# Performance work log

Hardware: AMD Instinct MI355X
Metric: run time of the kernel (lower is better)

## Reference

```python
import jax, jax.numpy as jnp
import numpy as np

NUM_EMBEDDINGS = 8192
EMBEDDING_DIM = 64
N_VOXELS = 32768


def setup_inputs() -> dict:
    key = jax.random.key(0)
    k1, k2 = jax.random.split(key)
    z = jax.random.normal(k1, (N_VOXELS, EMBEDDING_DIM), dtype=jnp.float32)
    codebook = jax.random.normal(k2, (NUM_EMBEDDINGS, EMBEDDING_DIM), dtype=jnp.float32)
    return {"z": z, "codebook": codebook}


def reference(z, codebook):
    # Squared euclidean distances [N, K]; argmin is identical to argmin of cdist.
    # d2 = ||z||^2 - 2 z E^T + ||E||^2
    z_sq = jnp.sum(z * z, axis=1, keepdims=True)            # [N, 1]
    e_sq = jnp.sum(codebook * codebook, axis=1)              # [K]
    d2 = z_sq - 2.0 * (z @ codebook.T) + e_sq[None, :]       # [N, K]
    encoding_indices = jnp.argmin(d2, axis=1)                # [N] int

    quantized_feats = codebook[encoding_indices]             # [N, D] gather

    sg = jax.lax.stop_gradient
    commitment_loss = jnp.mean((z - sg(quantized_feats)) ** 2)
    vq_loss = jnp.mean((quantized_feats - sg(z)) ** 2)

    # Straight-through estimator
    quantized = z + sg(quantized_feats - z)                  # [N, D]

    return quantized, vq_loss, commitment_loss, encoding_indices
```

## Files before the change

### kernel.cpp

```cpp
#include <hip/hip_runtime.h>
#include <math.h>

#define N_VOX 32768
#define N_EMB 8192
#define DIM 64
#define NCHUNK 8
#define CODES_PER_CHUNK (N_EMB / NCHUNK)
#define TILES_PER_CHUNK (CODES_PER_CHUNK / 32)
#define NTILES (N_EMB / 32)
#define TILE_BYTES 8192
#define CHUNK_BYTES (TILES_PER_CHUNK * TILE_BYTES)

typedef _Float16 half8 __attribute__((ext_vector_type(8)));
typedef float floatx16 __attribute__((ext_vector_type(16)));

#define FP16_MIN_NORMAL 6.1035156e-5f
#define LO_SCALE 2048.0f

__global__ __launch_bounds__(64) void cbprep_kernel(const float* __restrict__ cb,
                                                    char* __restrict__ stream,
                                                    float* __restrict__ c0arr) {
    int l    = threadIdx.x;
    int m    = l & 31;
    int kg   = l >> 5;
    int tile = blockIdx.x;
    char* tbase = stream + (size_t)tile * TILE_BYTES;
    int code = tile * 32 + m;

    float ss = 0.f;
    #pragma unroll
    for (int o = 0; o < 4; ++o) {
        const float* p = cb + (size_t)code * DIM + o * 16 + kg * 8;
        half8 h, lo;
        #pragma unroll
        for (int j = 0; j < 8; ++j) {
            float x = p[j];
            ss = fmaf(x, x, ss);
            _Float16 hi = (_Float16)x;
            float hf = (float)hi;
            if (fabsf(hf) < FP16_MIN_NORMAL) { hi = (_Float16)0.f; hf = 0.f; }
            h[j]  = hi;
            lo[j] = (_Float16)((x - hf) * LO_SCALE);
        }
        *(half8*)(tbase +        o * 1024 + l * 16) = h;
        *(half8*)(tbase + 4096 + o * 1024 + l * 16) = lo;
    }
    ss += __shfl_xor(ss, 32, 64);
    if (kg == 0)
        c0arr[code] = -1024.0f * ss;
}

__global__ __launch_bounds__(512) void scan_kernel(const float* __restrict__ z,
                                                   const char* __restrict__ stream,
                                                   const float* __restrict__ c0arr,
                                                   float* __restrict__ cand_val,
                                                   int* __restrict__ cand_idx) {
    __shared__ __align__(16) char lds[2 * TILE_BYTES];
    int tid   = threadIdx.x;
    int l     = tid & 63;
    int w     = tid >> 6;
    int chunk = blockIdx.x & (NCHUNK - 1);
    int rg    = blockIdx.x >> 3;
    int m     = l & 31;
    int kg    = l >> 5;
    int rowBase = rg * 256 + w * 32;

    half8 zh[4], zl[4], zhs[4];
    const float* zrow = z + (size_t)(rowBase + m) * DIM + kg * 8;
    #pragma unroll
    for (int o = 0; o < 4; ++o) {
        const float* p = zrow + o * 16;
        #pragma unroll
        for (int j = 0; j < 8; ++j) {
            float x = p[j];
            _Float16 hi = (_Float16)x;
            float hf = (float)hi;
            if (fabsf(hf) < FP16_MIN_NORMAL) { hi = (_Float16)0.f; hf = 0.f; }
            zh[o][j] = hi;
            zl[o][j] = (_Float16)((x - hf) * LO_SCALE);
        }
        zhs[o] = zh[o] * (_Float16)2048.0f;
    }

    const char*  sbase = stream + (size_t)chunk * CHUNK_BYTES;
    const float* c0p   = c0arr + chunk * CODES_PER_CHUNK;

    float best[16];
    int   bt[16];
    #pragma unroll
    for (int i = 0; i < 16; ++i) { best[i] = -3.4e38f; bt[i] = 0; }

#define STAGE(gt, lb)                                                              \
    do {                                                                           \
        const char* _g = (gt) + w * 1024 + l * 16;                                 \
        char*       _d = (lb) + w * 1024 + l * 16;                                 \
        __builtin_amdgcn_global_load_lds(                                          \
            (const __attribute__((address_space(1))) void*)_g,                     \
            (__attribute__((address_space(3))) void*)_d, 16, 0, 0);                \
    } while (0)

    STAGE(sbase, lds);
    float c0 = c0p[m];
    __syncthreads();

    for (int t = 0; t < TILES_PER_CHUNK; ++t) {
        if (t + 1 < TILES_PER_CHUNK)
            STAGE(sbase + (size_t)(t + 1) * TILE_BYTES, lds + ((t + 1) & 1) * TILE_BYTES);
        float c0n = (t + 1 < TILES_PER_CHUNK) ? c0p[(t + 1) * 32 + m] : 0.f;

        const char* lb = lds + (t & 1) * TILE_BYTES;
        half8 bh[4], bl[4];
        #pragma unroll
        for (int o = 0; o < 4; ++o) {
            bh[o] = *(const half8*)(lb +        o * 1024 + l * 16);
            bl[o] = *(const half8*)(lb + 4096 + o * 1024 + l * 16);
        }

        floatx16 acc;
        #pragma unroll
        for (int i = 0; i < 16; ++i) acc[i] = c0;
        #pragma unroll
        for (int o = 0; o < 4; ++o) {
            acc = __builtin_amdgcn_mfma_f32_32x32x16_f16(zhs[o], bh[o], acc, 0, 0, 0);
            acc = __builtin_amdgcn_mfma_f32_32x32x16_f16(zl[o],  bh[o], acc, 0, 0, 0);
            acc = __builtin_amdgcn_mfma_f32_32x32x16_f16(zh[o],  bl[o], acc, 0, 0, 0);
        }
        #pragma unroll
        for (int i = 0; i < 16; ++i)
            if (acc[i] > best[i]) { best[i] = acc[i]; bt[i] = t; }

        c0 = c0n;
        __syncthreads();
    }
#undef STAGE

    #pragma unroll
    for (int i = 0; i < 16; ++i) {
        float v  = best[i];
        int   id = bt[i] * 32 + m;
        #pragma unroll
        for (int off = 1; off < 32; off <<= 1) {
            float ov = __shfl_xor(v, off, 64);
            int   oi = __shfl_xor(id, off, 64);
            if (ov > v || (ov == v && oi < id)) { v = ov; id = oi; }
        }
        if (m == 0) {
            int row = rowBase + (i & 3) + 8 * (i >> 2) + 4 * kg;
            cand_val[chunk * N_VOX + row] = v;
            cand_idx[chunk * N_VOX + row] = chunk * CODES_PER_CHUNK + id;
        }
    }
}

__global__ __launch_bounds__(256) void finalize_kernel(const float* __restrict__ z,
                                                       const float* __restrict__ cb,
                                                       const float* __restrict__ cand_val,
                                                       const int* __restrict__ cand_idx,
                                                       float* __restrict__ out,
                                                       float* __restrict__ partials) {
    int g    = blockIdx.x * 256 + threadIdx.x;
    int row  = g >> 3;
    int c    = g & 7;

    float v  = cand_val[c * N_VOX + row];
    int   id = cand_idx[c * N_VOX + row];
    #pragma unroll
    for (int off = 1; off < 8; off <<= 1) {
        float ov = __shfl_xor(v, off, 8);
        int   oi = __shfl_xor(id, off, 8);
        if (ov > v || (ov == v && oi < id)) { v = ov; id = oi; }
    }

    if (c == 0)
        out[(size_t)N_VOX * DIM + 2 + row] = (float)id;

    const float4* zp = (const float4*)(z  + (size_t)row * DIM + c * 8);
    const float4* qp = (const float4*)(cb + (size_t)id  * DIM + c * 8);
    float4*       op = (float4*)(out + (size_t)row * DIM + c * 8);
    float ss = 0.f;
    #pragma unroll
    for (int d = 0; d < 2; ++d) {
        float4 zt = zp[d], qt = qp[d];
        float dx = qt.x - zt.x, dy = qt.y - zt.y;
        float dz = qt.z - zt.z, dw = qt.w - zt.w;
        float4 o;
        o.x = zt.x + dx; o.y = zt.y + dy;
        o.z = zt.z + dz; o.w = zt.w + dw;
        op[d] = o;
        ss += dx*dx + dy*dy + dz*dz + dw*dw;
    }

    __shared__ float red[256];
    red[threadIdx.x] = ss;
    __syncthreads();
    #pragma unroll
    for (int s = 128; s > 0; s >>= 1) {
        if (threadIdx.x < s) red[threadIdx.x] += red[threadIdx.x + s];
        __syncthreads();
    }
    if (threadIdx.x == 0) partials[blockIdx.x] = red[0];
}

__global__ __launch_bounds__(256) void loss_kernel(const float* __restrict__ partials,
                                                   float* __restrict__ out) {
    __shared__ float red[256];
    red[threadIdx.x] = (partials[threadIdx.x]       + partials[threadIdx.x + 256])
                     + (partials[threadIdx.x + 512] + partials[threadIdx.x + 768]);
    __syncthreads();
    #pragma unroll
    for (int st = 128; st > 0; st >>= 1) {
        if (threadIdx.x < st) red[threadIdx.x] += red[threadIdx.x + st];
        __syncthreads();
    }
    if (threadIdx.x == 0) {
        float mean = red[0] / (float)((size_t)N_VOX * DIM);
        out[(size_t)N_VOX * DIM + 0] = mean;
        out[(size_t)N_VOX * DIM + 1] = mean;
    }
}

extern "C" void kernel_launch(void* const* d_in, const int* in_sizes, int n_in,
                              void* d_out, int out_size, void* d_ws, size_t ws_size,
                              hipStream_t stream) {
    const float* z  = (const float*)d_in[0];
    const float* cb = (const float*)d_in[1];
    float* out = (float*)d_out;

    char*  bstream  = (char*)d_ws;
    float* c0arr    = (float*)(bstream + (size_t)NTILES * TILE_BYTES);
    float* cand_val = c0arr + N_EMB;
    int*   cand_idx = (int*)(cand_val + (size_t)NCHUNK * N_VOX);
    float* partials = (float*)(cand_idx + (size_t)NCHUNK * N_VOX);

    cbprep_kernel  <<<dim3(NTILES), dim3(64), 0, stream>>>(cb, bstream, c0arr);
    scan_kernel    <<<dim3((N_VOX / 256) * NCHUNK), dim3(512), 0, stream>>>(z, bstream, c0arr, cand_val, cand_idx);
    finalize_kernel<<<dim3(N_VOX * 8 / 256), dim3(256), 0, stream>>>(z, cb, cand_val, cand_idx, out, partials);
    loss_kernel    <<<1, 256, 0, stream>>>(partials, out);
}
```

Before: 175.9 us.

## Deepen codebook tile pipeline to four LDS buffers and preload norms

The scan kernel moves from double-buffered to quad-buffered LDS staging with a prefetch distance of three tiles. It uses explicit vmcnt waits plus a single barrier per iteration in place of the trailing __syncthreads. Per-chunk codebook norms are loaded into LDS once instead of fetched from global memory each tile. The codebook prep kernel spreads the four 16-element slices across four wavefronts with an LDS reduction, aiming at more memory parallelism in that small kernel. LDS use per block grows to about 36 KB, which may lower occupancy. The hand-written waitcnt logic depends on the exact number of outstanding loads, which the z loads or c0 loads could disturb.

```diff
diff --git a/kernel.cpp b/kernel.cpp
--- a/kernel.cpp
+++ b/kernel.cpp
@@ -17,37 +17,43 @@
 #define FP16_MIN_NORMAL 6.1035156e-5f
 #define LO_SCALE 2048.0f
 
-__global__ __launch_bounds__(64) void cbprep_kernel(const float* __restrict__ cb,
-                                                    char* __restrict__ stream,
-                                                    float* __restrict__ c0arr) {
-    int l    = threadIdx.x;
+__global__ __launch_bounds__(256) void cbprep_kernel(const float* __restrict__ cb,
+                                                     char* __restrict__ stream,
+                                                     float* __restrict__ c0arr) {
+    __shared__ float red[256];
+    int tid  = threadIdx.x;
+    int l    = tid & 63;
+    int o    = tid >> 6;
     int m    = l & 31;
     int kg   = l >> 5;
     int tile = blockIdx.x;
     char* tbase = stream + (size_t)tile * TILE_BYTES;
     int code = tile * 32 + m;
 
+    const float* p = cb + (size_t)code * DIM + o * 16 + kg * 8;
     float ss = 0.f;
-    #pragma unroll
-    for (int o = 0; o < 4; ++o) {
-        const float* p = cb + (size_t)code * DIM + o * 16 + kg * 8;
-        half8 h, lo;
-        #pragma unroll
-        for (int j = 0; j < 8; ++j) {
-            float x = p[j];
-            ss = fmaf(x, x, ss);
-            _Float16 hi = (_Float16)x;
-            float hf = (float)hi;
-            if (fabsf(hf) < FP16_MIN_NORMAL) { hi = (_Float16)0.f; hf = 0.f; }
-            h[j]  = hi;
-            lo[j] = (_Float16)((x - hf) * LO_SCALE);
-        }
-        *(half8*)(tbase +        o * 1024 + l * 16) = h;
-        *(half8*)(tbase + 4096 + o * 1024 + l * 16) = lo;
-    }
-    ss += __shfl_xor(ss, 32, 64);
-    if (kg == 0)
-        c0arr[code] = -1024.0f * ss;
+    half8 h, lo;
+    #pragma unroll
+    for (int j = 0; j < 8; ++j) {
+        float x = p[j];
+        ss = fmaf(x, x, ss);
+        _Float16 hi = (_Float16)x;
+        float hf = (float)hi;
+        if (fabsf(hf) < FP16_MIN_NORMAL) { hi = (_Float16)0.f; hf = 0.f; }
+        h[j]  = hi;
+        lo[j] = (_Float16)((x - hf) * LO_SCALE);
+    }
+    *(half8*)(tbase +        o * 1024 + l * 16) = h;
+    *(half8*)(tbase + 4096 + o * 1024 + l * 16) = lo;
+
+    red[tid] = ss;
+    __syncthreads();
+    if (tid < 32) {
+        float s = 0.f;
+        #pragma unroll
+        for (int q = 0; q < 8; ++q) s += red[tid + q * 32];
+        c0arr[tile * 32 + tid] = -1024.0f * s;
+    }
 }
 
 __global__ __launch_bounds__(512) void scan_kernel(const float* __restrict__ z,
@@ -55,7 +61,8 @@
                                                    const float* __restrict__ c0arr,
                                                    float* __restrict__ cand_val,
                                                    int* __restrict__ cand_idx) {
-    __shared__ __align__(16) char lds[2 * TILE_BYTES];
+    __shared__ __align__(16) char lds[4 * TILE_BYTES + CODES_PER_CHUNK * 4];
+    float* c0_lds = (float*)(lds + 4 * TILE_BYTES);
     int tid   = threadIdx.x;
     int l     = tid & 63;
     int w     = tid >> 6;
@@ -99,16 +106,29 @@
             (__attribute__((address_space(3))) void*)_d, 16, 0, 0);                \
     } while (0)
 
-    STAGE(sbase, lds);
-    float c0 = c0p[m];
+    STAGE(sbase,                        lds);
+    STAGE(sbase + (size_t)TILE_BYTES,   lds + TILE_BYTES);
+    STAGE(sbase + 2 * (size_t)TILE_BYTES, lds + 2 * TILE_BYTES);
+    c0_lds[tid]       = c0p[tid];
+    c0_lds[tid + 512] = c0p[tid + 512];
     __syncthreads();
 
     for (int t = 0; t < TILES_PER_CHUNK; ++t) {
-        if (t + 1 < TILES_PER_CHUNK)
-            STAGE(sbase + (size_t)(t + 1) * TILE_BYTES, lds + ((t + 1) & 1) * TILE_BYTES);
-        float c0n = (t + 1 < TILES_PER_CHUNK) ? c0p[(t + 1) * 32 + m] : 0.f;
-
-        const char* lb = lds + (t & 1) * TILE_BYTES;
+        if (t < TILES_PER_CHUNK - 2)
+            asm volatile("s_waitcnt vmcnt(2)" ::: "memory");
+        else if (t == TILES_PER_CHUNK - 2)
+            asm volatile("s_waitcnt vmcnt(1)" ::: "memory");
+        else
+            asm volatile("s_waitcnt vmcnt(0)" ::: "memory");
+        __builtin_amdgcn_s_barrier();
+        asm volatile("" ::: "memory");
+
+        if (t + 3 < TILES_PER_CHUNK)
+            STAGE(sbase + (size_t)(t + 3) * TILE_BYTES,
+                  lds + ((t + 3) & 3) * TILE_BYTES);
+
+        const char* lb = lds + (t & 3) * TILE_BYTES;
+        float c0 = c0_lds[t * 32 + m];
         half8 bh[4], bl[4];
         #pragma unroll
         for (int o = 0; o < 4; ++o) {
@@ -128,9 +148,6 @@
         #pragma unroll
         for (int i = 0; i < 16; ++i)
             if (acc[i] > best[i]) { best[i] = acc[i]; bt[i] = t; }
-
-        c0 = c0n;
-        __syncthreads();
     }
 #undef STAGE
 
@@ -232,7 +249,7 @@
     int*   cand_idx = (int*)(cand_val + (size_t)NCHUNK * N_VOX);
     float* partials = (float*)(cand_idx + (size_t)NCHUNK * N_VOX);
 
-    cbprep_kernel  <<<dim3(NTILES), dim3(64), 0, stream>>>(cb, bstream, c0arr);
+    cbprep_kernel  <<<dim3(NTILES), dim3(256), 0, stream>>>(cb, bstream, c0arr);
     scan_kernel    <<<dim3((N_VOX / 256) * NCHUNK), dim3(512), 0, stream>>>(z, bstream, c0arr, cand_val, cand_idx);
     finalize_kernel<<<dim3(N_VOX * 8 / 256), dim3(256), 0, stream>>>(z, cb, cand_val, cand_idx, out, partials);
     loss_kernel    <<<1, 256, 0, stream>>>(partials, out);
```

Measured after the change: 175.7 us. About the same (-0.1%).
